# Optimization experiments

Measured on AMD Instinct MI355X. Metric: run time of the kernel, lower is better.

The kernel has to match this reference:

```python
import jax, jax.numpy as jnp
import numpy as np

NUM_GRAPHS = 1024  # static number of segments for global_mean_pool


def setup_inputs() -> dict:
    key = jax.random.key(0)
    ks = jax.random.split(key, 16)
    N, E, F_IN, H = 100000, 1000000, 32, 64
    NUM_ATOM, NUM_ACT, L = 16, 8, 3
    s = 0.05
    x = jax.random.normal(ks[0], (N, F_IN), dtype=jnp.float32)
    edge_index = jax.random.randint(ks[1], (2, E), 0, N, dtype=jnp.int64)
    batch = jnp.sort(jax.random.randint(ks[2], (N,), 0, NUM_GRAPHS, dtype=jnp.int64))
    W_emb = jax.random.normal(ks[3], (F_IN, H), dtype=jnp.float32) * s
    b_emb = jnp.zeros((H,), dtype=jnp.float32)
    W_convs = jax.random.normal(ks[4], (L, H, H), dtype=jnp.float32) * s
    b_convs = jnp.zeros((L, H), dtype=jnp.float32)
    W_act = jax.random.normal(ks[5], (H, NUM_ACT), dtype=jnp.float32) * s
    b_act = jnp.zeros((NUM_ACT,), dtype=jnp.float32)
    W_tgt = jax.random.normal(ks[6], (H, 1), dtype=jnp.float32) * s
    b_tgt = jnp.zeros((1,), dtype=jnp.float32)
    W_atom = jax.random.normal(ks[7], (H, NUM_ATOM), dtype=jnp.float32) * s
    b_atom = jnp.zeros((NUM_ATOM,), dtype=jnp.float32)
    return {"x": x, "edge_index": edge_index, "batch": batch,
            "W_emb": W_emb, "b_emb": b_emb, "W_convs": W_convs, "b_convs": b_convs,
            "W_act": W_act, "b_act": b_act, "W_tgt": W_tgt, "b_tgt": b_tgt,
            "W_atom": W_atom, "b_atom": b_atom}


def reference(x, edge_index, batch, W_emb, b_emb, W_convs, b_convs,
              W_act, b_act, W_tgt, b_tgt, W_atom, b_atom):
    N = x.shape[0]
    # --- GCN normalization with self-loops (PyG GCNConv default) ---
    self_idx = jnp.arange(N, dtype=edge_index.dtype)
    src = jnp.concatenate([edge_index[0], self_idx])  # message source (row)
    dst = jnp.concatenate([edge_index[1], self_idx])  # aggregation target (col)
    ones_e = jnp.ones(src.shape[0], dtype=x.dtype)
    deg = jax.ops.segment_sum(ones_e, dst, num_segments=N)  # in-degree + self-loop
    dinv = jnp.where(deg > 0, jax.lax.rsqrt(deg), 0.0)
    norm = (dinv[src] * dinv[dst])[:, None]  # [E+N, 1]

    h = jax.nn.relu(x @ W_emb + b_emb)  # node embedding
    for i in range(W_convs.shape[0]):
        m = (h @ W_convs[i])[src] * norm            # gather + scale
        agg = jax.ops.segment_sum(m, dst, num_segments=N)  # scatter-add
        h = jax.nn.relu(agg + b_convs[i])

    # --- global mean pool over graphs ---
    cnt = jax.ops.segment_sum(jnp.ones(N, dtype=x.dtype), batch, num_segments=NUM_GRAPHS)
    pooled = jax.ops.segment_sum(h, batch, num_segments=NUM_GRAPHS)
    pooled = pooled / jnp.maximum(cnt, 1.0)[:, None]

    action_type_logits = pooled @ W_act + b_act            # [G, num_action_types]
    target_node_logits = (h @ W_tgt + b_tgt)[:, 0]         # [N]
    new_atom_type_logits = pooled @ W_atom + b_atom        # [G, num_atom_types]
    return (action_type_logits, target_node_logits, new_atom_type_logits, h)
```

## Files before the change

### kernel.cpp

```cpp
#include <hip/hip_runtime.h>
#include <hip/hip_fp16.h>

#define HD 64
#define FIN 32
#define NG 1024
#define STRIDE 64
#define SLOT0 4
#define DEGCAP 59
#define SH 72

#define BINW 128
#define NBMAX 1024
#define EPB 8192

typedef _Float16 f16x8 __attribute__((ext_vector_type(8)));
typedef float f32x4 __attribute__((ext_vector_type(4)));
typedef int i32x4 __attribute__((ext_vector_type(4)));

__device__ __forceinline__ int fmap(int jt, int c) {
    return (jt < 2) ? (2 * c + jt) : (32 + 2 * c + (jt - 2));
}

__device__ __forceinline__ void nt_store_h2(__half2 v, __half2* p) {
    __builtin_nontemporal_store(*(int*)&v, (int*)p);
}

__global__ __launch_bounds__(256) void k_prep(const int* __restrict__ dst,
                                              int* __restrict__ blkHist, int E, int NBINS,
                                              __half2* __restrict__ BaZR,
                                              __half2* __restrict__ BbZR,
                                              const float* __restrict__ Wconv,
                                              __half* __restrict__ Wf, int wtotal,
                                              const float* __restrict__ Wemb,
                                              __half* __restrict__ Wef) {
    __shared__ int hist[NBMAX];
    int b = blockIdx.x, t = threadIdx.x;
    if (b < 48) {
        int tid = b * 256 + t;
        if (tid < wtotal) {
            int layer = tid >> 12;
            int r = tid & 4095;
            int frag = r >> 9, lane = (r >> 3) & 63, e = r & 7;
            int jt = frag >> 1, kh = frag & 1;
            int k = kh * 32 + (lane >> 4) * 8 + e;
            int n = fmap(jt, lane & 15);
            Wf[tid] = (_Float16)Wconv[(size_t)layer * 4096 + k * 64 + n];
        }
    } else if (b < 56) {
        int tid = (b - 48) * 256 + t;
        if (tid < 2048) {
            int jt = tid >> 9, lane = (tid >> 3) & 63, e = tid & 7;
            int k = (lane >> 4) * 8 + e;
            int n = fmap(jt, lane & 15);
            Wef[tid] = (_Float16)Wemb[k * HD + n];
        }
    } else if (b == 56) {
        __half2 z = __floats2half2_rn(0.f, 0.f);
        if (t < 32) BaZR[t] = z;
        else if (t < 64) BbZR[t - 32] = z;
    }
    int e0 = b * EPB;
    if (e0 < E) {
        for (int i = t; i < NBMAX; i += 256) hist[i] = 0;
        __syncthreads();
        int e1 = e0 + EPB; if (e1 > E) e1 = E;
        for (int e = e0 + t; e < e1; e += 256) atomicAdd(&hist[dst[e] >> 7], 1);
        __syncthreads();
        for (int i = t; i < NBINS; i += 256) blkHist[b * NBMAX + i] = hist[i];
    }
}

__global__ __launch_bounds__(1024) void k_scan(int* __restrict__ blkHist,
                                               int* __restrict__ binStart,
                                               int nb, int NBINS) {
    __shared__ int s[NBMAX];
    int t = threadIdx.x;
    int run = 0;
    if (t < NBINS) {
        for (int blk = 0; blk < nb; blk++) {
            int x = blkHist[blk * NBMAX + t];
            blkHist[blk * NBMAX + t] = run;
            run += x;
        }
    }
    s[t] = run;
    __syncthreads();
    for (int off = 1; off < NBMAX; off <<= 1) {
        int v = s[t];
        int u = (t >= off) ? s[t - off] : 0;
        __syncthreads();
        s[t] = v + u;
        __syncthreads();
    }
    if (t <= NBINS) binStart[t] = (t == 0) ? 0 : s[t - 1];
}

__global__ __launch_bounds__(256) void k_scatter(const int* __restrict__ src,
                                                 const int* __restrict__ dst,
                                                 const int* __restrict__ blkHist,
                                                 const int* __restrict__ binStart,
                                                 int2* __restrict__ binned,
                                                 int E, int NBINS) {
    __shared__ int pos[NBMAX];
    int b = blockIdx.x, t = threadIdx.x;
    for (int i = t; i < NBMAX; i += 256)
        pos[i] = (i < NBINS) ? (blkHist[b * NBMAX + i] + binStart[i]) : 0;
    __syncthreads();
    int e0 = b * EPB;
    int e1 = e0 + EPB; if (e1 > E) e1 = E;
    for (int e = e0 + t; e < e1; e += 256) {
        int d = dst[e];
        int p = atomicAdd(&pos[d >> 7], 1);
        binned[p] = make_int2(src[e], d);
    }
}

__global__ __launch_bounds__(256) void k_csr(const int2* __restrict__ binned,
                                             const int* __restrict__ binStart,
                                             int* __restrict__ col, int N) {
    __shared__ int img[BINW * 64];
    __shared__ int cnt[BINW];
    int b = blockIdx.x, t = threadIdx.x;
    for (int i = t; i < BINW * 64; i += 256) img[i] = 0;
    for (int i = t; i < BINW; i += 256) cnt[i] = 0;
    __syncthreads();
    int s = binStart[b], e = binStart[b + 1];
    for (int i = s + t; i < e; i += 256) {
        int2 ed = binned[i];
        int ld = ed.y & (BINW - 1);
        int p = atomicAdd(&cnt[ld], 1);
        if (p < STRIDE - SLOT0) img[ld * 64 + SLOT0 + p] = ed.x;
    }
    __syncthreads();
    for (int i = t; i < BINW; i += 256) img[i * 64] = cnt[i];
    __syncthreads();
    int v0 = b * BINW;
    int* out = col + ((size_t)v0 << 6);
    for (int j = t; j < BINW * 16; j += 256) {
        int node = v0 + (j >> 4);
        if (node < N) {
            i32x4 val = *(i32x4*)&img[j * 4];
            __builtin_nontemporal_store(val, (i32x4*)(out + j * 4));
        }
    }
}

__device__ __forceinline__ void gemm_from_lds(const __half* hs, const float* dvs,
                                              const float4* __restrict__ Wf4,
                                              __half2* __restrict__ Bout,
                                              int node0, int N, int t) {
    int lane = t & 63;
    int wv = t >> 6;
    int lm = lane & 15, kq = lane >> 4;
    union U { float4 f; f16x8 h; };
    U a0, a1;
    const __half* hrow = hs + (size_t)(wv * 16 + lm) * SH;
    a0.f = *(const float4*)(hrow + kq * 8);
    a1.f = *(const float4*)(hrow + 32 + kq * 8);
    f32x4 acc[4];
#pragma unroll
    for (int jt = 0; jt < 4; jt++) acc[jt] = (f32x4){0.f, 0.f, 0.f, 0.f};
#pragma unroll
    for (int jt = 0; jt < 4; jt++) {
        U b0, b1;
        b0.f = Wf4[(jt * 2 + 0) * 64 + lane];
        b1.f = Wf4[(jt * 2 + 1) * 64 + lane];
        acc[jt] = __builtin_amdgcn_mfma_f32_16x16x32_f16(a0.h, b0.h, acc[jt], 0, 0, 0);
        acc[jt] = __builtin_amdgcn_mfma_f32_16x16x32_f16(a1.h, b1.h, acc[jt], 0, 0, 0);
    }
#pragma unroll
    for (int r = 0; r < 4; r++) {
        int lv = wv * 16 + kq * 4 + r;
        int v = node0 + lv;
        if (v < N) {
            float dv = dvs[lv];
            nt_store_h2(__floats2half2_rn(acc[0][r] * dv, acc[1][r] * dv),
                        Bout + (size_t)v * 32 + lm);
            nt_store_h2(__floats2half2_rn(acc[2][r] * dv, acc[3][r] * dv),
                        Bout + (size_t)v * 32 + 16 + lm);
        }
    }
}

__global__ __launch_bounds__(256) void k_emb_gemm0(const float* __restrict__ x,
                                                   const float4* __restrict__ Wef4,
                                                   const float* __restrict__ bemb,
                                                   const int* __restrict__ col,
                                                   const float4* __restrict__ Wf0,
                                                   __half2* __restrict__ Bout, int N) {
    __shared__ __half hs[64 * SH];
    __shared__ float dvs[64];
    int t = threadIdx.x;
    int lane = t & 63;
    int wv = t >> 6;
    int node0 = blockIdx.x * 64;
    int nodew = node0 + wv * 16;
    int m = lane & 15, kq = lane >> 4;

    int vm = nodew + m;
    if (vm > N - 1) vm = N - 1;
    const float4* xr = (const float4*)(x + (size_t)vm * FIN + kq * 8);
    float4 xa = xr[0], xb = xr[1];
    f16x8 a;
    a[0] = (_Float16)xa.x; a[1] = (_Float16)xa.y; a[2] = (_Float16)xa.z; a[3] = (_Float16)xa.w;
    a[4] = (_Float16)xb.x; a[5] = (_Float16)xb.y; a[6] = (_Float16)xb.z; a[7] = (_Float16)xb.w;

    union U { float4 f; f16x8 h; };
    f32x4 acc[4];
#pragma unroll
    for (int jt = 0; jt < 4; jt++) {
        U b; b.f = Wef4[jt * 64 + lane];
        acc[jt] = (f32x4){0.f, 0.f, 0.f, 0.f};
        acc[jt] = __builtin_amdgcn_mfma_f32_16x16x32_f16(a, b.h, acc[jt], 0, 0, 0);
    }
    float b01x = bemb[2 * m], b01y = bemb[2 * m + 1];
    float b23x = bemb[32 + 2 * m], b23y = bemb[32 + 2 * m + 1];
    __half2 z = __floats2half2_rn(0.f, 0.f);
#pragma unroll
    for (int r = 0; r < 4; r++) {
        int lv = wv * 16 + kq * 4 + r;
        int v = node0 + lv;
        __half2 p01 = z, p23 = z;
        if (v < N) {
            p01 = __floats2half2_rn(fmaxf(acc[0][r] + b01x, 0.f),
                                    fmaxf(acc[1][r] + b01y, 0.f));
            p23 = __floats2half2_rn(fmaxf(acc[2][r] + b23x, 0.f),
                                    fmaxf(acc[3][r] + b23y, 0.f));
        }
        *(__half2*)(hs + (size_t)lv * SH + 2 * m) = p01;
        *(__half2*)(hs + (size_t)lv * SH + 32 + 2 * m) = p23;
        if (m == 0)
            dvs[lv] = (v < N) ? rsqrtf((float)(col[(size_t)v << 6] + 1)) : 1.f;
    }
    __syncthreads();
    gemm_from_lds(hs, dvs, Wf0, Bout, node0, N, t);
}

__global__ __launch_bounds__(256) void k_layer(const __half2* __restrict__ Bin,
                                               const int* __restrict__ col,
                                               const float* __restrict__ bias,
                                               const float4* __restrict__ Wnext,
                                               __half2* __restrict__ Bout,
                                               int N, int ZR) {
    __shared__ __half hs[64 * SH];
    __shared__ float dvs[64];
    int t = threadIdx.x;
    int lane = t & 63;
    int wv = t >> 6;
    int node0 = blockIdx.x * 64;
    int q = lane >> 4, p = lane & 15;
    float4 b4 = *(const float4*)(bias + 4 * p);

#pragma unroll
    for (int pass = 0; pass < 4; pass++) {
        int lv = wv * 16 + pass * 4 + q;
        int v = node0 + lv;
        int vc = (v < N) ? v : 0;
        const int* bucket = col + ((size_t)vc << 6);
        int degraw = bucket[0];
        int deg = degraw > DEGCAP ? DEGCAP : degraw;
        int dmax = deg;
        dmax = max(dmax, __shfl_xor(dmax, 16, 64));
        dmax = max(dmax, __shfl_xor(dmax, 32, 64));
        int rounds = (dmax + 4) >> 2;

        float2 a0 = make_float2(0.f, 0.f), a1 = make_float2(0.f, 0.f);
        for (int rd = 0; rd < rounds; rd++) {
            int4 iq = *(const int4*)(bucket + SLOT0 + rd * 4);
            int idx[4] = {iq.x, iq.y, iq.z, iq.w};
#pragma unroll
            for (int r = 0; r < 4; r++) {
                int i = rd * 4 + r;
                idx[r] = (i < deg) ? idx[r] : ((i == deg) ? vc : ZR);
            }
            float2 raw[4];
#pragma unroll
            for (int r = 0; r < 4; r++)
                raw[r] = *(const float2*)(Bin + (size_t)idx[r] * 32 + p * 2);
#pragma unroll
            for (int r = 0; r < 4; r++) {
                float2 f0 = __half22float2(((const __half2*)&raw[r])[0]);
                float2 f1 = __half22float2(((const __half2*)&raw[r])[1]);
                a0.x += f0.x; a0.y += f0.y; a1.x += f1.x; a1.y += f1.y;
            }
        }
        float dv = rsqrtf((float)(degraw + 1));
        float r0 = fmaxf(dv * a0.x + b4.x, 0.f);
        float r1 = fmaxf(dv * a0.y + b4.y, 0.f);
        float r2 = fmaxf(dv * a1.x + b4.z, 0.f);
        float r3 = fmaxf(dv * a1.y + b4.w, 0.f);
        if (v >= N) { r0 = r1 = r2 = r3 = 0.f; dv = 1.f; }
        __half* hrow = hs + (size_t)lv * SH + 4 * p;
        *(__half2*)(hrow) = __floats2half2_rn(r0, r1);
        *(__half2*)(hrow + 2) = __floats2half2_rn(r2, r3);
        if (p == 0) dvs[lv] = dv;
    }
    __syncthreads();
    gemm_from_lds(hs, dvs, Wnext, Bout, node0, N, t);
}

__global__ __launch_bounds__(256) void k_gather_last(const __half2* __restrict__ Bin,
                                                     const int* __restrict__ col,
                                                     const float* __restrict__ bias,
                                                     float* __restrict__ hout,
                                                     const float* __restrict__ Wtgt,
                                                     const float* __restrict__ btgt,
                                                     float* __restrict__ tgt,
                                                     int N, int ZR) {
    int t = threadIdx.x;
    int lane = t & 63;
    int wv = t >> 6;
    int q = lane >> 4, p = lane & 15;
    int v = blockIdx.x * 16 + wv * 4 + q;
    if (v >= N) return;

    const int* bucket = col + ((size_t)v << 6);
    int degraw = bucket[0];
    int deg = degraw > DEGCAP ? DEGCAP : degraw;
    int dmax = deg;
    dmax = max(dmax, __shfl_xor(dmax, 16, 64));
    dmax = max(dmax, __shfl_xor(dmax, 32, 64));
    int rounds = (dmax + 4) >> 2;

    float2 a0 = make_float2(0.f, 0.f), a1 = make_float2(0.f, 0.f);
    for (int rd = 0; rd < rounds; rd++) {
        int4 iq = *(const int4*)(bucket + SLOT0 + rd * 4);
        int idx[4] = {iq.x, iq.y, iq.z, iq.w};
#pragma unroll
        for (int r = 0; r < 4; r++) {
            int i = rd * 4 + r;
            idx[r] = (i < deg) ? idx[r] : ((i == deg) ? v : ZR);
        }
        float2 raw[4];
#pragma unroll
        for (int r = 0; r < 4; r++)
            raw[r] = *(const float2*)(Bin + (size_t)idx[r] * 32 + p * 2);
#pragma unroll
        for (int r = 0; r < 4; r++) {
            float2 f0 = __half22float2(((const __half2*)&raw[r])[0]);
            float2 f1 = __half22float2(((const __half2*)&raw[r])[1]);
            a0.x += f0.x; a0.y += f0.y; a1.x += f1.x; a1.y += f1.y;
        }
    }
    float dv = rsqrtf((float)(degraw + 1));
    float4 b4 = *(const float4*)(bias + 4 * p);
    float r0 = fmaxf(dv * a0.x + b4.x, 0.f);
    float r1 = fmaxf(dv * a0.y + b4.y, 0.f);
    float r2 = fmaxf(dv * a1.x + b4.z, 0.f);
    float r3 = fmaxf(dv * a1.y + b4.w, 0.f);
    f32x4 o = (f32x4){r0, r1, r2, r3};
    __builtin_nontemporal_store(o, (f32x4*)(hout + (size_t)v * HD + 4 * p));
    float4 w4 = *(const float4*)(Wtgt + 4 * p);
    float pp = r0 * w4.x + r1 * w4.y + r2 * w4.z + r3 * w4.w;
    pp += __shfl_xor(pp, 1, 64); pp += __shfl_xor(pp, 2, 64);
    pp += __shfl_xor(pp, 4, 64); pp += __shfl_xor(pp, 8, 64);
    if (p == 0) __builtin_nontemporal_store(pp + btgt[0], tgt + v);
}

__global__ __launch_bounds__(256) void k_pool(const float* __restrict__ h,
                                              const int* __restrict__ batch,
                                              const float* __restrict__ Wact,
                                              const float* __restrict__ bact,
                                              const float* __restrict__ Watom,
                                              const float* __restrict__ batom,
                                              float* __restrict__ out_act,
                                              float* __restrict__ out_atom, int N) {
    int g = blockIdx.x;
    int t = threadIdx.x;
    int q = t >> 4, p = t & 15;
    int lo = 0, hi = N;
    while (lo < hi) { int mid = (lo + hi) >> 1; if (batch[mid] < g) lo = mid + 1; else hi = mid; }
    int s = lo;
    hi = N;
    while (lo < hi) { int mid = (lo + hi) >> 1; if (batch[mid] < g + 1) lo = mid + 1; else hi = mid; }
    int e2 = lo;
    float4 acc = make_float4(0.f, 0.f, 0.f, 0.f);
    for (int v = s + q; v < e2; v += 16) {
        float4 c = *(const float4*)(h + (size_t)v * HD + p * 4);
        acc.x += c.x; acc.y += c.y; acc.z += c.z; acc.w += c.w;
    }
    __shared__ float4 part[16][16];
    part[q][p] = acc;
    __syncthreads();
    __shared__ float pl[HD];
    if (t < 16) {
        float4 tot = part[0][t];
#pragma unroll
        for (int k = 1; k < 16; k++) {
            float4 c = part[k][t];
            tot.x += c.x; tot.y += c.y; tot.z += c.z; tot.w += c.w;
        }
        float cnt = fmaxf((float)(e2 - s), 1.f);
        pl[t * 4 + 0] = tot.x / cnt; pl[t * 4 + 1] = tot.y / cnt;
        pl[t * 4 + 2] = tot.z / cnt; pl[t * 4 + 3] = tot.w / cnt;
    }
    __syncthreads();
    if (t < 8) {
        float a = bact[t];
#pragma unroll
        for (int k = 0; k < HD; k++) a += pl[k] * Wact[k * 8 + t];
        out_act[g * 8 + t] = a;
    }
    if (t < 16) {
        float a = batom[t];
#pragma unroll
        for (int k = 0; k < HD; k++) a += pl[k] * Watom[k * 16 + t];
        out_atom[g * 16 + t] = a;
    }
}

extern "C" void kernel_launch(void* const* d_in, const int* in_sizes, int n_in,
                              void* d_out, int out_size, void* d_ws, size_t ws_size,
                              hipStream_t stream) {
    const float* x     = (const float*)d_in[0];
    const int*   ei    = (const int*)d_in[1];
    const int*   batch = (const int*)d_in[2];
    const float* Wemb  = (const float*)d_in[3];
    const float* bemb  = (const float*)d_in[4];
    const float* Wconv = (const float*)d_in[5];
    const float* bconv = (const float*)d_in[6];
    const float* Wact  = (const float*)d_in[7];
    const float* bact  = (const float*)d_in[8];
    const float* Wtgt  = (const float*)d_in[9];
    const float* btgt  = (const float*)d_in[10];
    const float* Watom = (const float*)d_in[11];
    const float* batom = (const float*)d_in[12];

    const int N = in_sizes[0] / FIN;
    const int E = in_sizes[1] / 2;
    const int L = in_sizes[5] / (HD * HD);
    const int Npad = (N + 63) & ~63;
    const int ZR = Npad;

    int*     col = (int*)d_ws;
    __half2* Ba  = (__half2*)(col + ((size_t)N << 6));
    __half2* Bb  = Ba + (size_t)(Npad + 64) * 32;
    __half*  Wf  = (__half*)(Bb + (size_t)(Npad + 64) * 32);
    __half*  Wef = Wf + (size_t)L * 4096;

    int2* binned   = (int2*)Bb;
    int*  blkHist  = (int*)((char*)Bb + (9u << 20));
    int*  binStart = (int*)((char*)Bb + (10u << 20) + (512u << 10));

    const int* srcA = ei;
    const int* dstA = ei + E;

    float* out_act  = (float*)d_out;
    float* out_tgt  = out_act + (size_t)NG * 8;
    float* out_atom = out_tgt + N;
    float* out_h    = out_atom + (size_t)NG * 16;

    const int nbG = (N + 63) / 64;
    const int nbLast = (N + 15) / 16;
    const int wtotal = L * 4096;
    const int nbF1 = (E + EPB - 1) / EPB;
    const int NBINS = (N + BINW - 1) / BINW;
    const int nbPrep = nbF1 > 57 ? nbF1 : 57;

    k_prep<<<nbPrep, 256, 0, stream>>>(dstA, blkHist, E, NBINS,
                                       Ba + (size_t)ZR * 32, Bb + (size_t)ZR * 32,
                                       Wconv, Wf, wtotal, Wemb, Wef);
    k_scan<<<1, 1024, 0, stream>>>(blkHist, binStart, nbF1, NBINS);
    k_scatter<<<nbF1, 256, 0, stream>>>(srcA, dstA, blkHist, binStart, binned, E, NBINS);
    k_csr<<<NBINS, 256, 0, stream>>>(binned, binStart, col, N);
    k_emb_gemm0<<<nbG, 256, 0, stream>>>(x, (const float4*)Wef, bemb, col,
                                         (const float4*)Wf, Ba, N);

    __half2* cur = Ba;
    __half2* nxt = Bb;
    for (int l = 0; l < L - 1; ++l) {
        k_layer<<<nbG, 256, 0, stream>>>(cur, col, bconv + l * HD,
                                         (const float4*)(Wf + (size_t)(l + 1) * 4096),
                                         nxt, N, ZR);
        __half2* tmp = cur; cur = nxt; nxt = tmp;
    }
    k_gather_last<<<nbLast, 256, 0, stream>>>(cur, col, bconv + (size_t)(L - 1) * HD,
                                              out_h, Wtgt, btgt, out_tgt, N, ZR);
    k_pool<<<NG, 256, 0, stream>>>(out_h, batch, Wact, bact, Watom, batom,
                                   out_act, out_atom, N);
}
```

Before: 265.6 us.

## Replace serial per-bin block scan with global atomic bin offsets and pack edges

```diff
diff --git a/kernel.cpp b/kernel.cpp
--- a/kernel.cpp
+++ b/kernel.cpp
@@ -12,6 +12,7 @@
 #define BINW 128
 #define NBMAX 1024
 #define EPB 8192
+#define BCS 16
 
 typedef _Float16 f16x8 __attribute__((ext_vector_type(8)));
 typedef float f32x4 __attribute__((ext_vector_type(4)));
@@ -25,8 +26,15 @@
     __builtin_nontemporal_store(*(int*)&v, (int*)p);
 }
 
+__global__ __launch_bounds__(256) void k_zero(int* __restrict__ binCnt, int n) {
+    int i = blockIdx.x * 256 + threadIdx.x;
+    if (i < n) binCnt[i] = 0;
+}
+
 __global__ __launch_bounds__(256) void k_prep(const int* __restrict__ dst,
-                                              int* __restrict__ blkHist, int E, int NBINS,
+                                              int* __restrict__ blkBase,
+                                              int* __restrict__ binCnt,
+                                              int E, int NBINS,
                                               __half2* __restrict__ BaZR,
                                               __half2* __restrict__ BbZR,
                                               const float* __restrict__ Wconv,
@@ -66,24 +74,18 @@
         int e1 = e0 + EPB; if (e1 > E) e1 = E;
         for (int e = e0 + t; e < e1; e += 256) atomicAdd(&hist[dst[e] >> 7], 1);
         __syncthreads();
-        for (int i = t; i < NBINS; i += 256) blkHist[b * NBMAX + i] = hist[i];
-    }
-}
-
-__global__ __launch_bounds__(1024) void k_scan(int* __restrict__ blkHist,
-                                               int* __restrict__ binStart,
-                                               int nb, int NBINS) {
+        for (int i = t; i < NBINS; i += 256) {
+            int h = hist[i];
+            if (h) blkBase[b * NBMAX + i] = atomicAdd(&binCnt[i * BCS], h);
+        }
+    }
+}
+
+__global__ __launch_bounds__(1024) void k_scanlite(const int* __restrict__ binCnt,
+                                                   int* __restrict__ binStart, int NBINS) {
     __shared__ int s[NBMAX];
     int t = threadIdx.x;
-    int run = 0;
-    if (t < NBINS) {
-        for (int blk = 0; blk < nb; blk++) {
-            int x = blkHist[blk * NBMAX + t];
-            blkHist[blk * NBMAX + t] = run;
-            run += x;
-        }
-    }
-    s[t] = run;
+    s[t] = (t < NBINS) ? binCnt[t * BCS] : 0;
     __syncthreads();
     for (int off = 1; off < NBMAX; off <<= 1) {
         int v = s[t];
@@ -92,30 +94,35 @@
         s[t] = v + u;
         __syncthreads();
     }
-    if (t <= NBINS) binStart[t] = (t == 0) ? 0 : s[t - 1];
+    if (t == 0) binStart[0] = 0;
+    binStart[t + 1] = s[t];
 }
 
 __global__ __launch_bounds__(256) void k_scatter(const int* __restrict__ src,
                                                  const int* __restrict__ dst,
-                                                 const int* __restrict__ blkHist,
+                                                 const int* __restrict__ blkBase,
                                                  const int* __restrict__ binStart,
-                                                 int2* __restrict__ binned,
+                                                 int* __restrict__ binned,
                                                  int E, int NBINS) {
-    __shared__ int pos[NBMAX];
+    __shared__ int base[NBMAX];
+    __shared__ int lpos[NBMAX];
     int b = blockIdx.x, t = threadIdx.x;
-    for (int i = t; i < NBMAX; i += 256)
-        pos[i] = (i < NBINS) ? (blkHist[b * NBMAX + i] + binStart[i]) : 0;
+    for (int i = t; i < NBMAX; i += 256) {
+        lpos[i] = 0;
+        base[i] = (i < NBINS) ? (binStart[i] + blkBase[b * NBMAX + i]) : 0;
+    }
     __syncthreads();
     int e0 = b * EPB;
     int e1 = e0 + EPB; if (e1 > E) e1 = E;
     for (int e = e0 + t; e < e1; e += 256) {
         int d = dst[e];
-        int p = atomicAdd(&pos[d >> 7], 1);
-        binned[p] = make_int2(src[e], d);
-    }
-}
-
-__global__ __launch_bounds__(256) void k_csr(const int2* __restrict__ binned,
+        int bin = d >> 7;
+        int p = base[bin] + atomicAdd(&lpos[bin], 1);
+        binned[p] = (src[e] << 7) | (d & (BINW - 1));
+    }
+}
+
+__global__ __launch_bounds__(256) void k_csr(const int* __restrict__ binned,
                                              const int* __restrict__ binStart,
                                              int* __restrict__ col, int N) {
     __shared__ int img[BINW * 64];
@@ -126,10 +133,10 @@
     __syncthreads();
     int s = binStart[b], e = binStart[b + 1];
     for (int i = s + t; i < e; i += 256) {
-        int2 ed = binned[i];
-        int ld = ed.y & (BINW - 1);
+        int w = binned[i];
+        int ld = w & (BINW - 1);
         int p = atomicAdd(&cnt[ld], 1);
-        if (p < STRIDE - SLOT0) img[ld * 64 + SLOT0 + p] = ed.x;
+        if (p < STRIDE - SLOT0) img[ld * 64 + SLOT0 + p] = (int)((unsigned)w >> 7);
     }
     __syncthreads();
     for (int i = t; i < BINW; i += 256) img[i * 64] = cnt[i];
@@ -438,9 +445,10 @@
     __half*  Wf  = (__half*)(Bb + (size_t)(Npad + 64) * 32);
     __half*  Wef = Wf + (size_t)L * 4096;
 
-    int2* binned   = (int2*)Bb;
-    int*  blkHist  = (int*)((char*)Bb + (9u << 20));
-    int*  binStart = (int*)((char*)Bb + (10u << 20) + (512u << 10));
+    int* binned   = (int*)Bb;
+    int* blkBase  = (int*)((char*)Bb + (8u << 20));
+    int* binCnt   = (int*)((char*)Bb + (9u << 20));
+    int* binStart = (int*)((char*)Bb + (9u << 20) + (256u << 10));
 
     const int* srcA = ei;
     const int* dstA = ei + E;
@@ -456,12 +464,14 @@
     const int nbF1 = (E + EPB - 1) / EPB;
     const int NBINS = (N + BINW - 1) / BINW;
     const int nbPrep = nbF1 > 57 ? nbF1 : 57;
-
-    k_prep<<<nbPrep, 256, 0, stream>>>(dstA, blkHist, E, NBINS,
+    const int nZero = NBMAX * BCS;
+
+    k_zero<<<(nZero + 255) / 256, 256, 0, stream>>>(binCnt, nZero);
+    k_prep<<<nbPrep, 256, 0, stream>>>(dstA, blkBase, binCnt, E, NBINS,
                                        Ba + (size_t)ZR * 32, Bb + (size_t)ZR * 32,
                                        Wconv, Wf, wtotal, Wemb, Wef);
-    k_scan<<<1, 1024, 0, stream>>>(blkHist, binStart, nbF1, NBINS);
-    k_scatter<<<nbF1, 256, 0, stream>>>(srcA, dstA, blkHist, binStart, binned, E, NBINS);
+    k_scanlite<<<1, 1024, 0, stream>>>(binCnt, binStart, NBINS);
+    k_scatter<<<nbF1, 256, 0, stream>>>(srcA, dstA, blkBase, binStart, binned, E, NBINS);
     k_csr<<<NBINS, 256, 0, stream>>>(binned, binStart, col, N);
     k_emb_gemm0<<<nbG, 256, 0, stream>>>(x, (const float4*)Wef, bemb, col,
                                          (const float4*)Wf, Ba, N);
```

Result: faster. 242.0 us (-8.9%).
